# Kernel optimization log

Measured on AMD Instinct MI355X. Metric: run time of the kernel, lower is better.

Reference implementation:

```python
import jax, jax.numpy as jnp
import numpy as np

B, S, Hd = 2, 2048, 2048
NH, DH = 16, 128
FF = 4 * Hd
EPS = 1e-5


def layer_norm(x, g, b):
    mu = jnp.mean(x, axis=-1, keepdims=True)
    var = jnp.mean(jnp.square(x - mu), axis=-1, keepdims=True)
    return (x - mu) * jax.lax.rsqrt(var + EPS) * g + b


def setup_inputs() -> dict:
    key = jax.random.key(0)
    ks = jax.random.split(key, 10)
    s = lambda n: 1.0 / np.sqrt(n)
    return {
        "hidden_states": jax.random.normal(ks[0], (B, S, Hd), jnp.float32),
        "attention_mask": jnp.zeros((B, S), jnp.float32),
        "ln1_g": jnp.ones((Hd,), jnp.float32),
        "ln1_b": jnp.zeros((Hd,), jnp.float32),
        "ln2_g": jnp.ones((Hd,), jnp.float32),
        "ln2_b": jnp.zeros((Hd,), jnp.float32),
        "Wq": jax.random.normal(ks[1], (Hd, NH * DH), jnp.float32) * s(Hd),
        "Wk": jax.random.normal(ks[2], (Hd, NH * DH), jnp.float32) * s(Hd),
        "Wv": jax.random.normal(ks[3], (Hd, NH * DH), jnp.float32) * s(Hd),
        "Wo": jax.random.normal(ks[4], (NH * DH, Hd), jnp.float32) * s(NH * DH),
        "W1": jax.random.normal(ks[5], (Hd, FF), jnp.float32) * s(Hd),
        "b1": jnp.zeros((FF,), jnp.float32),
        "W2": jax.random.normal(ks[6], (FF, Hd), jnp.float32) * s(FF),
        "b2": jnp.zeros((Hd,), jnp.float32),
    }


def reference(hidden_states, attention_mask, ln1_g, ln1_b, ln2_g, ln2_b,
              Wq, Wk, Wv, Wo, W1, b1, W2, b2):
    x = hidden_states
    # --- attention sub-block ---
    h = layer_norm(x, ln1_g, ln1_b)
    q = (h @ Wq).reshape(B, S, NH, DH)
    k = (h @ Wk).reshape(B, S, NH, DH)
    v = (h @ Wv).reshape(B, S, NH, DH)
    scores = jnp.einsum("bqhd,bkhd->bhqk", q, k) / np.sqrt(DH).astype(np.float32)
    scores = scores + attention_mask[:, None, None, :]  # additive mask
    probs = jax.nn.softmax(scores, axis=-1)
    ctx = jnp.einsum("bhqk,bkhd->bqhd", probs, v).reshape(B, S, NH * DH)
    x = x + ctx @ Wo
    # --- MLP sub-block ---
    h = layer_norm(x, ln2_g, ln2_b)
    h = jax.nn.gelu(h @ W1 + b1, approximate=False)
    x = x + h @ W2 + b2
    return x
```

## Files before the change

### kernel.cpp

```cpp
#include <hip/hip_runtime.h>
#include <math.h>

#define B_ 2
#define S_ 2048
#define HD 2048
#define NH_ 16
#define DH_ 128
#define FF_ 8192
#define MROWS (B_*S_)
#define LDQ 6144

typedef __attribute__((ext_vector_type(8))) short bf16x8;
typedef __attribute__((ext_vector_type(4))) short s16x4;
typedef __attribute__((ext_vector_type(4))) float f32x4;

static __device__ __forceinline__ unsigned short f2bf(float f) {
    unsigned u = __float_as_uint(f);
    u += 0x7fffu + ((u >> 16) & 1u);
    return (unsigned short)(u >> 16);
}

static __device__ __forceinline__ unsigned short f2bf_rna(float f) {
    return (unsigned short)((__float_as_uint(f) + 0x8000u) >> 16);
}

static __device__ __forceinline__ void gload_lds16(const void* g, void* lds) {
    __builtin_amdgcn_global_load_lds((const __attribute__((address_space(1))) void*)g,
                                     (__attribute__((address_space(3))) void*)lds, 16, 0, 0);
}

__global__ __launch_bounds__(256) void trcvt_kernel(const float* __restrict__ W,
        short* __restrict__ Wt, int K, int N) {
    __shared__ float tile[64][65];
    int t = threadIdx.x;
    int tr = t >> 4;
    int tc4 = (t & 15) * 4;
    int r0 = blockIdx.y * 64, c0 = blockIdx.x * 64;
    #pragma unroll
    for (int i = 0; i < 4; i++) {
        float4 v = *(const float4*)(W + (size_t)(r0 + tr + 16*i) * N + c0 + tc4);
        tile[tr + 16*i][tc4 + 0] = v.x;
        tile[tr + 16*i][tc4 + 1] = v.y;
        tile[tr + 16*i][tc4 + 2] = v.z;
        tile[tr + 16*i][tc4 + 3] = v.w;
    }
    __syncthreads();
    #pragma unroll
    for (int i = 0; i < 4; i++) {
        int oc = tr + 16*i;
        s16x4 o;
        o.x = (short)f2bf(tile[tc4 + 0][oc]);
        o.y = (short)f2bf(tile[tc4 + 1][oc]);
        o.z = (short)f2bf(tile[tc4 + 2][oc]);
        o.w = (short)f2bf(tile[tc4 + 3][oc]);
        *(s16x4*)(Wt + (size_t)(c0 + oc) * K + r0 + tc4) = o;
    }
}

__global__ __launch_bounds__(256) void vtrans_kernel(const short* __restrict__ qkv,
        short* __restrict__ vT) {
    __shared__ short tile[32][33];
    int t = threadIdx.x;
    int tx = t & 31, ty = t >> 5;
    int c0 = blockIdx.x * 32;
    int r0 = blockIdx.y * 32;
    int b  = blockIdx.z;
    #pragma unroll
    for (int i = 0; i < 4; i++)
        tile[ty + 8*i][tx] = qkv[(size_t)(b*S_ + r0 + ty + 8*i) * LDQ + 4096 + c0 + tx];
    __syncthreads();
    #pragma unroll
    for (int i = 0; i < 4; i++)
        vT[((size_t)(c0 + ty + 8*i) * 2 + b) * S_ + r0 + tx] = tile[tx][ty + 8*i];
}

__global__ __launch_bounds__(256) void ln_kernel(const float* __restrict__ x,
                const float* __restrict__ g, const float* __restrict__ b,
                short* __restrict__ out) {
    int row = blockIdx.x;
    const float* xr = x + (size_t)row * HD;
    short* orow = out + (size_t)row * HD;
    int t = threadIdx.x;

    float4 v0 = ((const float4*)xr)[t];
    float4 v1 = ((const float4*)xr)[t + 256];
    float s  = v0.x + v0.y + v0.z + v0.w + v1.x + v1.y + v1.z + v1.w;
    float ss = v0.x*v0.x + v0.y*v0.y + v0.z*v0.z + v0.w*v0.w
             + v1.x*v1.x + v1.y*v1.y + v1.z*v1.z + v1.w*v1.w;

    #pragma unroll
    for (int off = 1; off < 64; off <<= 1) {
        s  += __shfl_xor(s,  off, 64);
        ss += __shfl_xor(ss, off, 64);
    }
    __shared__ float ws_s[4], ws_q[4];
    int wid = t >> 6;
    if ((t & 63) == 0) { ws_s[wid] = s; ws_q[wid] = ss; }
    __syncthreads();
    s  = ws_s[0] + ws_s[1] + ws_s[2] + ws_s[3];
    ss = ws_q[0] + ws_q[1] + ws_q[2] + ws_q[3];

    float mu  = s * (1.0f / HD);
    float var = ss * (1.0f / HD) - mu * mu;
    float rs  = rsqrtf(var + 1e-5f);

    float4 g0 = ((const float4*)g)[t];
    float4 g1 = ((const float4*)g)[t + 256];
    float4 b0 = ((const float4*)b)[t];
    float4 b1 = ((const float4*)b)[t + 256];
    s16x4 o0, o1;
    o0.x = (short)f2bf((v0.x - mu) * rs * g0.x + b0.x);
    o0.y = (short)f2bf((v0.y - mu) * rs * g0.y + b0.y);
    o0.z = (short)f2bf((v0.z - mu) * rs * g0.z + b0.z);
    o0.w = (short)f2bf((v0.w - mu) * rs * g0.w + b0.w);
    o1.x = (short)f2bf((v1.x - mu) * rs * g1.x + b1.x);
    o1.y = (short)f2bf((v1.y - mu) * rs * g1.y + b1.y);
    o1.z = (short)f2bf((v1.z - mu) * rs * g1.z + b1.z);
    o1.w = (short)f2bf((v1.w - mu) * rs * g1.w + b1.w);
    ((s16x4*)orow)[t]       = o0;
    ((s16x4*)orow)[t + 256] = o1;
}

template<bool PATCH, bool OUTBF16, bool BIAS, bool RES, bool GELU>
__global__ __launch_bounds__(256, 2) void gemm128(
        const short* __restrict__ A, const short* __restrict__ Bt,
        const float* __restrict__ bias, const float* __restrict__ res,
        void* __restrict__ Cout, int M, int N, int K) {
    __shared__ __align__(16) char ldsA[2][128 * 128];
    __shared__ __align__(16) char ldsB[2][128 * 128];

    int tid = threadIdx.x;
    int wave = tid >> 6, lane = tid & 63;
    int l4 = lane >> 4, lm = lane & 15;
    int wm = wave >> 1, wn = wave & 1;

    int bid = blockIdx.x;
    int m0, n0;
    if constexpr (PATCH) {
        int xcd = bid & 7, local = bid >> 3;
        m0 = ((xcd & 3) * 8 + (local & 7)) << 7;
        n0 = ((xcd >> 2) * 8 + (local >> 3)) << 7;
    } else {
        int nx = N >> 7;
        m0 = (bid / nx) << 7; n0 = (bid % nx) << 7;
    }

    const short* Atile = A + (size_t)m0 * K;
    const short* Btile = Bt + (size_t)n0 * K;
    const int NT = K >> 6;

    auto stage = [&](int t, int buf) {
        int tw = (t >= NT) ? t - NT : t;
        const short* gA = Atile + tw * 64;
        const short* gB = Btile + tw * 64;
        #pragma unroll
        for (int s = 0; s < 4; s++) {
            int n = (wave * 4 + s) * 64 + lane;
            int row = n >> 3, c = n & 7;
            int cs = c ^ (row & 7);
            gload_lds16(gA + (size_t)row * K + cs * 8, ldsA[buf] + n * 16);
            gload_lds16(gB + (size_t)row * K + cs * 8, ldsB[buf] + n * 16);
        }
    };

    int ch0 = (l4) ^ (lm & 7);
    int ch1 = (4 | l4) ^ (lm & 7);
    const char* pA = (const char*)ldsA + (wm * 64 + lm) * 128;
    const char* pB = (const char*)ldsB + (wn * 64 + lm) * 128;

    f32x4 acc[4][4] = {};

    stage(0, 0);
    for (int t = 0; t < NT; t++) {
        int buf = t & 1;
        stage(t + 1, buf ^ 1);
        asm volatile("s_waitcnt vmcnt(8)" ::: "memory");
        __builtin_amdgcn_s_barrier();
        __builtin_amdgcn_sched_barrier(0);
        size_t bo = (size_t)buf * 128 * 128;
        __builtin_amdgcn_s_setprio(1);
        #pragma unroll
        for (int kk = 0; kk < 2; kk++) {
            int ch = kk ? ch1 : ch0;
            bf16x8 av[4], bv[4];
            #pragma unroll
            for (int f = 0; f < 4; f++)
                av[f] = *(const bf16x8*)(pA + bo + f * 2048 + ch * 16);
            #pragma unroll
            for (int nn = 0; nn < 4; nn++)
                bv[nn] = *(const bf16x8*)(pB + bo + nn * 2048 + ch * 16);
            #pragma unroll
            for (int f = 0; f < 4; f++)
                #pragma unroll
                for (int nn = 0; nn < 4; nn++)
                    acc[f][nn] = __builtin_amdgcn_mfma_f32_16x16x32_bf16(
                        av[f], bv[nn], acc[f][nn], 0, 0, 0);
        }
        __builtin_amdgcn_s_setprio(0);
        __builtin_amdgcn_s_barrier();
    }
    asm volatile("s_waitcnt vmcnt(0)" ::: "memory");
    __builtin_amdgcn_s_barrier();

    #pragma unroll
    for (int nn = 0; nn < 4; nn++) {
        int colb = n0 + wn * 64 + nn * 16 + lm;
        float bvs = BIAS ? bias[colb] : 0.f;
        #pragma unroll
        for (int m = 0; m < 4; m++) {
            #pragma unroll
            for (int r = 0; r < 4; r++) {
                int row = m0 + wm * 64 + m * 16 + l4 * 4 + r;
                float v = acc[m][nn][r] + bvs;
                if (GELU) {
                    float y = 1.5957691f * (v + 0.044715f * v * v * v);
                    v = v / (1.0f + __expf(-y));
                }
                size_t off = (size_t)row * N + colb;
                if (RES) v += res[off];
                if (OUTBF16) ((short*)Cout)[off] = (short)f2bf(v);
                else         ((float*)Cout)[off] = v;
            }
        }
    }
}

__global__ __launch_bounds__(256) void attn_kernel(
        const short* __restrict__ qkv, const short* __restrict__ vT,
        const float* __restrict__ mask, short* __restrict__ ctx) {
    __shared__ __align__(16) short Ks[2][64*128];
    __shared__ __align__(16) short Vt[2][128*64];
    __shared__ __align__(16) short Ps[4][16*72];
    int t = threadIdx.x;
    int wave = t >> 6, lane = t & 63;
    int l4 = lane >> 4, lm = lane & 15;
    int q0 = blockIdx.x * 64, h = blockIdx.y, zb = blockIdx.z;
    const float scale = 0.08838834764831845f;
    const int NT = S_ / 64;

    bf16x8 aq[4];
    {
        const short* qrow = qkv + (size_t)(zb*S_ + q0 + wave*16 + lm) * LDQ + h*DH_;
        #pragma unroll
        for (int ks = 0; ks < 4; ks++)
            aq[ks] = *(const bf16x8*)(qrow + ks*32 + l4*8);
    }

    auto stageKV = [&](int ti, int buf) {
        int tw = (ti >= NT) ? ti - NT : ti;
        int kv0 = tw * 64;
        #pragma unroll
        for (int L = 0; L < 4; L++) {
            int c = (wave*4 + L)*64 + lane;
            int krow = c >> 4, kc = c & 15;
            int ksrc = (kc & 8) | ((kc ^ (krow & 7)) & 7);
            gload_lds16(qkv + (size_t)(zb*S_ + kv0 + krow)*LDQ + 2048 + h*DH_ + ksrc*8,
                        (char*)Ks[buf] + c*16);
            int drow = c >> 3, dc = c & 7;
            int dsrc = dc ^ (drow & 7);
            gload_lds16(vT + ((size_t)(h*DH_ + drow)*2 + zb)*S_ + kv0 + dsrc*8,
                        (char*)Vt[buf] + c*16);
        }
    };

    float m_r[4], l_r[4];
    #pragma unroll
    for (int r = 0; r < 4; r++) { m_r[r] = -INFINITY; l_r[r] = 0.f; }
    f32x4 o[8];
    #pragma unroll
    for (int i = 0; i < 8; i++) o[i] = (f32x4){0.f, 0.f, 0.f, 0.f};

    stageKV(0, 0);
    for (int ti = 0; ti < NT; ti++) {
        int buf = ti & 1;
        int kv0 = ti * 64;
        stageKV(ti + 1, buf ^ 1);
        asm volatile("s_waitcnt vmcnt(8)" ::: "memory");
        __builtin_amdgcn_s_barrier();
        __builtin_amdgcn_sched_barrier(0);
        const char* Kb = (const char*)Ks[buf];
        const char* Vb = (const char*)Vt[buf];

        f32x4 s[4];
        #pragma unroll
        for (int nb = 0; nb < 4; nb++) s[nb] = (f32x4){0.f, 0.f, 0.f, 0.f};
        __builtin_amdgcn_s_setprio(1);
        #pragma unroll
        for (int nb = 0; nb < 4; nb++) {
            int row = nb*16 + lm;
            #pragma unroll
            for (int ks = 0; ks < 4; ks++) {
                bf16x8 bk = *(const bf16x8*)(Kb +
                              ((row*256 + ks*64 + l4*16) ^ ((row & 7) << 4)));
                s[nb] = __builtin_amdgcn_mfma_f32_16x16x32_bf16(aq[ks], bk, s[nb], 0, 0, 0);
            }
        }
        __builtin_amdgcn_s_setprio(0);

        float mk[4];
        #pragma unroll
        for (int nb = 0; nb < 4; nb++) mk[nb] = mask[(size_t)zb*S_ + kv0 + nb*16 + lm];

        float pv_[4][4], pm[4];
        float need = -1e30f;
        #pragma unroll
        for (int r = 0; r < 4; r++) {
            float vmax = -INFINITY;
            #pragma unroll
            for (int nb = 0; nb < 4; nb++) {
                float v = fmaf(s[nb][r], scale, mk[nb]);
                pv_[r][nb] = v;
                vmax = fmaxf(vmax, v);
            }
            vmax = fmaxf(vmax, __shfl_xor(vmax, 1, 64));
            vmax = fmaxf(vmax, __shfl_xor(vmax, 2, 64));
            vmax = fmaxf(vmax, __shfl_xor(vmax, 4, 64));
            vmax = fmaxf(vmax, __shfl_xor(vmax, 8, 64));
            pm[r] = vmax;
            need = fmaxf(need, vmax - m_r[r]);
        }
        if (!__all(need <= 8.0f)) {
            float fac[4];
            #pragma unroll
            for (int r = 0; r < 4; r++) {
                float nm = fmaxf(m_r[r], pm[r]);
                fac[r] = __expf(m_r[r] - nm);
                l_r[r] *= fac[r];
                m_r[r] = nm;
            }
            #pragma unroll
            for (int i = 0; i < 8; i++)
                #pragma unroll
                for (int r = 0; r < 4; r++) o[i][r] *= fac[r];
        }
        #pragma unroll
        for (int r = 0; r < 4; r++) {
            float ps = 0.f;
            #pragma unroll
            for (int nb = 0; nb < 4; nb++) {
                float e = __expf(pv_[r][nb] - m_r[r]);
                pv_[r][nb] = e;
                ps += e;
            }
            ps += __shfl_xor(ps, 1, 64);
            ps += __shfl_xor(ps, 2, 64);
            ps += __shfl_xor(ps, 4, 64);
            ps += __shfl_xor(ps, 8, 64);
            l_r[r] += ps;
        }

        short* Pw = (short*)Ps[wave];
        #pragma unroll
        for (int r = 0; r < 4; r++)
            #pragma unroll
            for (int nb = 0; nb < 4; nb++)
                Pw[(l4*4 + r)*72 + nb*16 + lm] = (short)f2bf_rna(pv_[r][nb]);

        __builtin_amdgcn_s_setprio(1);
        #pragma unroll
        for (int ks = 0; ks < 2; ks++) {
            bf16x8 ap = *(const bf16x8*)(Pw + lm*72 + ks*32 + l4*8);
            #pragma unroll
            for (int nd = 0; nd < 8; nd++) {
                int d = nd*16 + lm;
                bf16x8 bvv = *(const bf16x8*)(Vb +
                              (((d*128) + ks*64 + l4*16) ^ ((d & 7) << 4)));
                o[nd] = __builtin_amdgcn_mfma_f32_16x16x32_bf16(ap, bvv, o[nd], 0, 0, 0);
            }
        }
        __builtin_amdgcn_s_setprio(0);
        __builtin_amdgcn_s_barrier();
    }
    asm volatile("s_waitcnt vmcnt(0)" ::: "memory");
    __builtin_amdgcn_s_barrier();

    float inv[4];
    #pragma unroll
    for (int r = 0; r < 4; r++) inv[r] = 1.0f / l_r[r];
    #pragma unroll
    for (int nd = 0; nd < 8; nd++) {
        #pragma unroll
        for (int r = 0; r < 4; r++) {
            size_t row = (size_t)(zb*S_ + q0 + wave*16 + l4*4 + r);
            ctx[row * HD + h*DH_ + nd*16 + lm] = (short)f2bf(o[nd][r] * inv[r]);
        }
    }
}

extern "C" void kernel_launch(void* const* d_in, const int* in_sizes, int n_in,
                              void* d_out, int out_size, void* d_ws, size_t ws_size,
                              hipStream_t stream) {
    const float* x      = (const float*)d_in[0];
    const float* mask   = (const float*)d_in[1];
    const float* ln1_g  = (const float*)d_in[2];
    const float* ln1_b  = (const float*)d_in[3];
    const float* ln2_g  = (const float*)d_in[4];
    const float* ln2_b  = (const float*)d_in[5];
    const float* Wq     = (const float*)d_in[6];
    const float* Wk     = (const float*)d_in[7];
    const float* Wv     = (const float*)d_in[8];
    const float* Wo     = (const float*)d_in[9];
    const float* W1     = (const float*)d_in[10];
    const float* b1     = (const float*)d_in[11];
    const float* W2     = (const float*)d_in[12];
    const float* b2     = (const float*)d_in[13];
    float* out = (float*)d_out;

    char* ws = (char*)d_ws;
    size_t off = 0;
    const size_t WSQ  = (size_t)HD * HD * 2;
    const size_t WFF  = (size_t)HD * FF_ * 2;
    const size_t ACTB = (size_t)MROWS * HD * 2;
    short* WqkvT = (short*)(ws + off); off += 3 * WSQ;
    short* WoT   = (short*)(ws + off); off += WSQ;
    short* W1T   = (short*)(ws + off); off += WFF;
    short* W2T   = (short*)(ws + off); off += WFF;
    short* hb    = (short*)(ws + off); off += ACTB;
    short* qkv   = (short*)(ws + off); off += (size_t)MROWS * LDQ * 2;
    short* vTb   = (short*)(ws + off); off += (size_t)HD * B_ * S_ * 2;
    float* x1    = (float*)(ws + off); off += (size_t)MROWS * HD * 4;
    short* cb    = WqkvT;
    short* act   = qkv;

    dim3 blk(256);

    trcvt_kernel<<<dim3(HD/64,  HD/64),  blk, 0, stream>>>(Wq, WqkvT,                 HD, HD);
    trcvt_kernel<<<dim3(HD/64,  HD/64),  blk, 0, stream>>>(Wk, WqkvT + (size_t)HD*HD, HD, HD);
    trcvt_kernel<<<dim3(HD/64,  HD/64),  blk, 0, stream>>>(Wv, WqkvT + (size_t)2*HD*HD, HD, HD);
    trcvt_kernel<<<dim3(HD/64,  HD/64),  blk, 0, stream>>>(Wo, WoT, HD, HD);
    trcvt_kernel<<<dim3(FF_/64, HD/64),  blk, 0, stream>>>(W1, W1T, HD, FF_);
    trcvt_kernel<<<dim3(HD/64,  FF_/64), blk, 0, stream>>>(W2, W2T, FF_, HD);

    ln_kernel<<<MROWS, blk, 0, stream>>>(x, ln1_g, ln1_b, hb);

    gemm128<false,true,false,false,false><<<dim3((MROWS/128)*(LDQ/128)), 256, 0, stream>>>(
        hb, WqkvT, nullptr, nullptr, qkv, MROWS, LDQ, HD);

    vtrans_kernel<<<dim3(HD/32, S_/32, B_), blk, 0, stream>>>(qkv, vTb);

    attn_kernel<<<dim3(S_/64, NH_, B_), blk, 0, stream>>>(qkv, vTb, mask, cb);

    gemm128<true,false,false,true,false><<<dim3((MROWS/128)*(HD/128)), 256, 0, stream>>>(
        cb, WoT, nullptr, x, x1, MROWS, HD, HD);

    ln_kernel<<<MROWS, blk, 0, stream>>>(x1, ln2_g, ln2_b, hb);

    gemm128<false,true,true,false,true><<<dim3((MROWS/128)*(FF_/128)), 256, 0, stream>>>(
        hb, W1T, b1, nullptr, act, MROWS, FF_, HD);

    gemm128<true,false,true,true,false><<<dim3((MROWS/128)*(HD/128)), 256, 0, stream>>>(
        act, W2T, b2, x1, out, MROWS, HD, FF_);
}
```

Before: 765.4 us.

## Use wave-wide running max and MFMA row sums in flash attention softmax

Replaces the per-row running max with one running max per wave, shared by all 16 query rows, so one butterfly reduction and a scalar rescale factor replace four. Row sums now come from an extra MFMA of the bf16 probabilities against a ones vector instead of shuffle reductions. The P tile in LDS gets an XOR swizzle to reduce bank conflicts. The shared max risks precision loss or underflow when rows in a wave have very different maxima, and the row sums now use bf16-rounded probabilities.

After: 745.1 us (median of 2 runs). -2.6%, faster.

```diff
diff --git a/kernel.cpp b/kernel.cpp
--- a/kernel.cpp
+++ b/kernel.cpp
@@ -245,6 +245,9 @@
         for (int ks = 0; ks < 4; ks++)
             aq[ks] = *(const bf16x8*)(qrow + ks*32 + l4*8);
     }
+    bf16x8 onesb;
+    #pragma unroll
+    for (int i = 0; i < 8; i++) onesb[i] = (short)0x3F80;
 
     auto stageKV = [&](int ti, int buf) {
         int tw = (ti >= NT) ? ti - NT : ti;
@@ -263,9 +266,8 @@
         }
     };
 
-    float m_r[4], l_r[4];
-    #pragma unroll
-    for (int r = 0; r < 4; r++) { m_r[r] = -INFINITY; l_r[r] = 0.f; }
+    float m_run = -INFINITY;
+    f32x4 lsum = (f32x4){0.f, 0.f, 0.f, 0.f};
     f32x4 o[8];
     #pragma unroll
     for (int i = 0; i < 8; i++) o[i] = (f32x4){0.f, 0.f, 0.f, 0.f};
@@ -301,65 +303,55 @@
         #pragma unroll
         for (int nb = 0; nb < 4; nb++) mk[nb] = mask[(size_t)zb*S_ + kv0 + nb*16 + lm];
 
-        float pv_[4][4], pm[4];
-        float need = -1e30f;
-        #pragma unroll
-        for (int r = 0; r < 4; r++) {
-            float vmax = -INFINITY;
+        float pv_[4][4];
+        float vmax = -INFINITY;
+        #pragma unroll
+        for (int r = 0; r < 4; r++)
             #pragma unroll
             for (int nb = 0; nb < 4; nb++) {
                 float v = fmaf(s[nb][r], scale, mk[nb]);
                 pv_[r][nb] = v;
                 vmax = fmaxf(vmax, v);
             }
-            vmax = fmaxf(vmax, __shfl_xor(vmax, 1, 64));
-            vmax = fmaxf(vmax, __shfl_xor(vmax, 2, 64));
-            vmax = fmaxf(vmax, __shfl_xor(vmax, 4, 64));
-            vmax = fmaxf(vmax, __shfl_xor(vmax, 8, 64));
-            pm[r] = vmax;
-            need = fmaxf(need, vmax - m_r[r]);
-        }
-        if (!__all(need <= 8.0f)) {
-            float fac[4];
-            #pragma unroll
-            for (int r = 0; r < 4; r++) {
-                float nm = fmaxf(m_r[r], pm[r]);
-                fac[r] = __expf(m_r[r] - nm);
-                l_r[r] *= fac[r];
-                m_r[r] = nm;
-            }
+        vmax = fmaxf(vmax, __shfl_xor(vmax, 1, 64));
+        vmax = fmaxf(vmax, __shfl_xor(vmax, 2, 64));
+        vmax = fmaxf(vmax, __shfl_xor(vmax, 4, 64));
+        vmax = fmaxf(vmax, __shfl_xor(vmax, 8, 64));
+        vmax = fmaxf(vmax, __shfl_xor(vmax, 16, 64));
+        vmax = fmaxf(vmax, __shfl_xor(vmax, 32, 64));
+        if (!__all(vmax - m_run <= 8.0f)) {
+            float nm = fmaxf(m_run, vmax);
+            float fac = __expf(m_run - nm);
+            m_run = nm;
+            #pragma unroll
+            for (int r = 0; r < 4; r++) lsum[r] *= fac;
             #pragma unroll
             for (int i = 0; i < 8; i++)
                 #pragma unroll
-                for (int r = 0; r < 4; r++) o[i][r] *= fac[r];
-        }
+                for (int r = 0; r < 4; r++) o[i][r] *= fac;
+        }
+        #pragma unroll
+        for (int r = 0; r < 4; r++)
+            #pragma unroll
+            for (int nb = 0; nb < 4; nb++)
+                pv_[r][nb] = __expf(pv_[r][nb] - m_run);
+
+        char* Pw = (char*)Ps[wave];
         #pragma unroll
         for (int r = 0; r < 4; r++) {
-            float ps = 0.f;
-            #pragma unroll
-            for (int nb = 0; nb < 4; nb++) {
-                float e = __expf(pv_[r][nb] - m_r[r]);
-                pv_[r][nb] = e;
-                ps += e;
-            }
-            ps += __shfl_xor(ps, 1, 64);
-            ps += __shfl_xor(ps, 2, 64);
-            ps += __shfl_xor(ps, 4, 64);
-            ps += __shfl_xor(ps, 8, 64);
-            l_r[r] += ps;
-        }
-
-        short* Pw = (short*)Ps[wave];
-        #pragma unroll
-        for (int r = 0; r < 4; r++)
+            int rowb = (l4*4 + r) * 144;
             #pragma unroll
             for (int nb = 0; nb < 4; nb++)
-                Pw[(l4*4 + r)*72 + nb*16 + lm] = (short)f2bf_rna(pv_[r][nb]);
+                *(short*)(Pw + rowb + (((nb*16 + lm)*2) ^ (l4 << 4))) =
+                    (short)f2bf_rna(pv_[r][nb]);
+        }
 
         __builtin_amdgcn_s_setprio(1);
         #pragma unroll
         for (int ks = 0; ks < 2; ks++) {
-            bf16x8 ap = *(const bf16x8*)(Pw + lm*72 + ks*32 + l4*8);
+            bf16x8 ap = *(const bf16x8*)(Pw + lm*144 +
+                          ((ks*64 + l4*16) ^ ((lm & 12) << 2)));
+            lsum = __builtin_amdgcn_mfma_f32_16x16x32_bf16(ap, onesb, lsum, 0, 0, 0);
             #pragma unroll
             for (int nd = 0; nd < 8; nd++) {
                 int d = nd*16 + lm;
@@ -376,7 +368,7 @@
 
     float inv[4];
     #pragma unroll
-    for (int r = 0; r < 4; r++) inv[r] = 1.0f / l_r[r];
+    for (int r = 0; r < 4; r++) inv[r] = 1.0f / lsum[r];
     #pragma unroll
     for (int nd = 0; nd < 8; nd++) {
         #pragma unroll
```
